# Kernel optimization log

Hardware: AMD Instinct MI355X
Metric: run time of the kernel (lower is better)

## Reference

```python
import jax, jax.numpy as jnp
import numpy as np

W_LOSS = 10.0
THRESHOLD = 1.0
ACOS_EPS = 1e-7


def _normalize(v, eps=1e-8):
    n = jnp.linalg.norm(v, axis=-1, keepdims=True)
    return v / jnp.maximum(n, eps)


def quat_to_rotmat(q):
    # q: (..., 4) in (w, x, y, z) order, as in Zhou et al. / EPN repo
    q = _normalize(q)
    w, x, y, z = q[..., 0], q[..., 1], q[..., 2], q[..., 3]
    R = jnp.stack([
        1 - 2 * (y * y + z * z), 2 * (x * y - z * w), 2 * (x * z + y * w),
        2 * (x * y + z * w), 1 - 2 * (x * x + z * z), 2 * (y * z - x * w),
        2 * (x * z - y * w), 2 * (y * z + x * w), 1 - 2 * (x * x + y * y),
    ], axis=-1)
    return R.reshape(q.shape[:-1] + (3, 3))


def acos_safe(x):
    return jnp.arccos(jnp.clip(x, -1.0 + ACOS_EPS, 1.0 - ACOS_EPS))


def angle_from_R(R):
    # R: (..., 3, 3) -> geodesic angle via trace
    tr = jnp.trace(R, axis1=-2, axis2=-1)
    return acos_safe(0.5 * (tr - 1.0))


def setup_inputs() -> dict:
    key = jax.random.key(0)
    k1, k2, k3, k4, k5 = jax.random.split(key, 5)
    B, NA, NR = 32768, 60, 4
    wts = jax.random.normal(k1, (B, NA), dtype=jnp.float32)
    label = jax.random.randint(k2, (B,), 0, NA, dtype=jnp.int64)
    y = jax.random.normal(k3, (B, NR, NA), dtype=jnp.float32)
    # gt_R and anchors are valid rotation matrices (via random quaternions)
    gt_R = quat_to_rotmat(jax.random.normal(k4, (B, NA, 4), dtype=jnp.float32))
    anchors = quat_to_rotmat(jax.random.normal(k5, (NA, 4), dtype=jnp.float32))
    return {"wts": wts, "label": label, "y": y, "gt_R": gt_R, "anchors": anchors}


def reference(wts, label, y, gt_R, anchors):
    b, na = wts.shape
    nr = y.shape[1]
    true_R = gt_R[:, 29]  # (b, 3, 3)

    # --- CrossEntropyLoss branch (classifier) ---
    logp = jax.nn.log_softmax(wts, axis=1)
    cls_loss = -jnp.mean(jnp.take_along_axis(logp, label[:, None], axis=1))
    preds = jnp.argmax(wts, axis=1)  # (b,)
    r_acc = jnp.mean((preds == label).astype(jnp.float32))

    # --- anchor-wise predicted rotations ---
    # y (b, nr, na) -> (b, na, nr) -> (b, na, 3, 3)
    pred_RAnchor = quat_to_rotmat(jnp.swapaxes(y, 1, 2))

    gt_bias = angle_from_R(gt_R)  # (b, na)
    mask = (gt_bias < THRESHOLD).astype(gt_R.dtype)[:, :, None, None]
    l2_loss = jnp.sum(jnp.square(gt_R * mask - pred_RAnchor * mask))
    loss = cls_loss + W_LOSS * l2_loss

    # --- final predicted rotation: gather best anchor, compose with anchor rot ---
    sel = jnp.take_along_axis(pred_RAnchor, preds[:, None, None, None], axis=1)[:, 0]  # (b,3,3)
    pred_R = jnp.einsum('bij,bjk->bik', anchors[preds], sel)

    # --- mean angular error ---
    ang_err = angle_from_R(jnp.einsum('bij,bkj->bik', pred_R, true_R))  # (b,)

    return (loss, cls_loss, W_LOSS * l2_loss, r_acc, ang_err)
```

## Files before the change

kernel.cpp:

```cpp
#include <hip/hip_runtime.h>
#include <math.h>

constexpr int Bc  = 32768;
constexpr int NAc = 60;
constexpr int NRc = 4;

constexpr int NP     = Bc * NAc;
constexpr int TILE   = 256;
constexpr int NTILES = NP / TILE;
constexpr int K1_BLOCKS = 3840;
constexpr int K2_BLOCKS = 1024;
constexpr int K2_WAVES  = K2_BLOCKS * 4;

#define COS_ONE 0.5403023058681398f

__global__ __launch_bounds__(256) void l2_pairs(
    const float* __restrict__ y,
    const float* __restrict__ gt_R,
    float*       __restrict__ l2p)
{
    __shared__ float4 sg4[TILE * 9 / 4];
    float* sg = (float*)sg4;
    const int tid = threadIdx.x;

    float acc = 0.0f;

    for (int tile = blockIdx.x; tile < NTILES; tile += gridDim.x) {
        __syncthreads();
        const float4* gbase = (const float4*)(gt_R + (size_t)tile * (TILE * 9));
        for (int i = tid; i < TILE * 9 / 4; i += 256) sg4[i] = gbase[i];
        __syncthreads();

        const int p = tile * TILE + tid;
        const int b = p / NAc;
        const int a = p - b * NAc;

        const float* yb = y + (size_t)b * (NRc * NAc) + a;
        float qw = yb[0 * NAc];
        float qx = yb[1 * NAc];
        float qy = yb[2 * NAc];
        float qz = yb[3 * NAc];

        const float* g = sg + tid * 9;
        float g0 = g[0], g1 = g[1], g2 = g[2];
        float g3 = g[3], g4 = g[4], g5 = g[5];
        float g6 = g[6], g7 = g[7], g8 = g[8];

        float n   = sqrtf(qw * qw + qx * qx + qy * qy + qz * qz);
        float inv = 1.0f / fmaxf(n, 1e-8f);
        qw *= inv; qx *= inv; qy *= inv; qz *= inv;

        float R00 = 1.0f - 2.0f * (qy * qy + qz * qz);
        float R01 = 2.0f * (qx * qy - qz * qw);
        float R02 = 2.0f * (qx * qz + qy * qw);
        float R10 = 2.0f * (qx * qy + qz * qw);
        float R11 = 1.0f - 2.0f * (qx * qx + qz * qz);
        float R12 = 2.0f * (qy * qz - qx * qw);
        float R20 = 2.0f * (qx * qz - qy * qw);
        float R21 = 2.0f * (qy * qz + qx * qw);
        float R22 = 1.0f - 2.0f * (qx * qx + qy * qy);

        float xb = 0.5f * (g0 + g4 + g8 - 1.0f);
        if (xb > COS_ONE) {
            float d0 = g0 - R00, d1 = g1 - R01, d2 = g2 - R02;
            float d3 = g3 - R10, d4 = g4 - R11, d5 = g5 - R12;
            float d6 = g6 - R20, d7 = g7 - R21, d8 = g8 - R22;
            acc += d0 * d0 + d1 * d1 + d2 * d2
                 + d3 * d3 + d4 * d4 + d5 * d5
                 + d6 * d6 + d7 * d7 + d8 * d8;
        }
    }

    for (int off = 32; off; off >>= 1) acc += __shfl_xor(acc, off, 64);
    __shared__ float sred[4];
    const int lane = tid & 63, wave = tid >> 6;
    if (lane == 0) sred[wave] = acc;
    __syncthreads();
    if (tid == 0) l2p[blockIdx.x] = sred[0] + sred[1] + sred[2] + sred[3];
}

__global__ __launch_bounds__(256) void cls_angerr(
    const float* __restrict__ wts,
    const int*   __restrict__ label,
    const float* __restrict__ y,
    const float* __restrict__ gt_R,
    const float* __restrict__ anchors,
    float*       __restrict__ out,
    float*       __restrict__ lpp,
    float*       __restrict__ crp)
{
    const int lane = threadIdx.x & 63;
    const int wave = threadIdx.x >> 6;
    const int gw   = blockIdx.x * 4 + wave;

    float lp_acc = 0.0f;
    float cr_acc = 0.0f;

    for (int b = gw; b < Bc; b += K2_WAVES) {
        float w = -INFINITY;
        if (lane < NAc) w = wts[(size_t)b * NAc + lane];
        float mv = w;
        int   mi = lane;
        for (int off = 32; off; off >>= 1) {
            float ov = __shfl_xor(mv, off, 64);
            int   oi = __shfl_xor(mi, off, 64);
            if (ov > mv || (ov == mv && oi < mi)) { mv = ov; mi = oi; }
        }
        float e  = (lane < NAc) ? expf(w - mv) : 0.0f;
        float se = e;
        for (int off = 32; off; off >>= 1) se += __shfl_xor(se, off, 64);
        float lse  = mv + logf(se);
        int   lab  = label[b];
        float wlab = __shfl(w, lab, 64);
        if (lane == 0) {
            lp_acc += wlab - lse;
            cr_acc += (mi == lab) ? 1.0f : 0.0f;
        }

        if (lane == mi) {
            const float* yb = y + (size_t)b * (NRc * NAc) + mi;
            float qw = yb[0 * NAc];
            float qx = yb[1 * NAc];
            float qy = yb[2 * NAc];
            float qz = yb[3 * NAc];
            float n   = sqrtf(qw * qw + qx * qx + qy * qy + qz * qz);
            float inv = 1.0f / fmaxf(n, 1e-8f);
            qw *= inv; qx *= inv; qy *= inv; qz *= inv;
            float R00 = 1.0f - 2.0f * (qy * qy + qz * qz);
            float R01 = 2.0f * (qx * qy - qz * qw);
            float R02 = 2.0f * (qx * qz + qy * qw);
            float R10 = 2.0f * (qx * qy + qz * qw);
            float R11 = 1.0f - 2.0f * (qx * qx + qz * qz);
            float R12 = 2.0f * (qy * qz - qx * qw);
            float R20 = 2.0f * (qx * qz - qy * qw);
            float R21 = 2.0f * (qy * qz + qx * qw);
            float R22 = 1.0f - 2.0f * (qx * qx + qy * qy);

            const float* A = anchors + (size_t)mi * 9;
            float a0 = A[0], a1 = A[1], a2 = A[2];
            float a3 = A[3], a4 = A[4], a5 = A[5];
            float a6 = A[6], a7 = A[7], a8 = A[8];
            float P00 = a0 * R00 + a1 * R10 + a2 * R20;
            float P01 = a0 * R01 + a1 * R11 + a2 * R21;
            float P02 = a0 * R02 + a1 * R12 + a2 * R22;
            float P10 = a3 * R00 + a4 * R10 + a5 * R20;
            float P11 = a3 * R01 + a4 * R11 + a5 * R21;
            float P12 = a3 * R02 + a4 * R12 + a5 * R22;
            float P20 = a6 * R00 + a7 * R10 + a8 * R20;
            float P21 = a6 * R01 + a7 * R11 + a8 * R21;
            float P22 = a6 * R02 + a7 * R12 + a8 * R22;
            const float* tR = gt_R + ((size_t)b * NAc + 29) * 9;
            float tr = P00 * tR[0] + P01 * tR[1] + P02 * tR[2]
                     + P10 * tR[3] + P11 * tR[4] + P12 * tR[5]
                     + P20 * tR[6] + P21 * tR[7] + P22 * tR[8];
            float cx = 0.5f * (tr - 1.0f);
            cx = fminf(fmaxf(cx, -1.0f + 1e-7f), 1.0f - 1e-7f);
            out[4 + b] = acosf(cx);
        }
    }

    for (int off = 32; off; off >>= 1) {
        lp_acc += __shfl_xor(lp_acc, off, 64);
        cr_acc += __shfl_xor(cr_acc, off, 64);
    }
    __shared__ float s_lp[4], s_cr[4];
    if (lane == 0) { s_lp[wave] = lp_acc; s_cr[wave] = cr_acc; }
    __syncthreads();
    if (threadIdx.x == 0) {
        lpp[blockIdx.x] = s_lp[0] + s_lp[1] + s_lp[2] + s_lp[3];
        crp[blockIdx.x] = s_cr[0] + s_cr[1] + s_cr[2] + s_cr[3];
    }
}

__global__ __launch_bounds__(64) void mtl_final(
    const float* __restrict__ l2p,
    const float* __restrict__ lpp,
    const float* __restrict__ crp,
    float*       __restrict__ out)
{
    const int lane = threadIdx.x;
    double l2 = 0.0, lp = 0.0, cr = 0.0;
    for (int i = lane; i < K1_BLOCKS; i += 64) l2 += (double)l2p[i];
    for (int i = lane; i < K2_BLOCKS; i += 64) {
        lp += (double)lpp[i];
        cr += (double)crp[i];
    }
    for (int off = 32; off; off >>= 1) {
        l2 += __shfl_xor(l2, off, 64);
        lp += __shfl_xor(lp, off, 64);
        cr += __shfl_xor(cr, off, 64);
    }
    if (lane == 0) {
        float cls = (float)(-lp / (double)Bc);
        float l2s = (float)(10.0 * l2);
        out[0] = cls + l2s;
        out[1] = cls;
        out[2] = l2s;
        out[3] = (float)(cr / (double)Bc);
    }
}

extern "C" void kernel_launch(void* const* d_in, const int* in_sizes, int n_in,
                              void* d_out, int out_size, void* d_ws, size_t ws_size,
                              hipStream_t stream) {
    const float* wts     = (const float*)d_in[0];
    const int*   label   = (const int*)d_in[1];
    const float* y       = (const float*)d_in[2];
    const float* gt_R    = (const float*)d_in[3];
    const float* anchors = (const float*)d_in[4];
    float* out = (float*)d_out;

    float* l2p = (float*)d_ws;
    float* lpp = l2p + K1_BLOCKS;
    float* crp = lpp + K2_BLOCKS;

    l2_pairs  <<<K1_BLOCKS, 256, 0, stream>>>(y, gt_R, l2p);
    cls_angerr<<<K2_BLOCKS, 256, 0, stream>>>(wts, label, y, gt_R, anchors, out, lpp, crp);
    mtl_final <<<1, 64, 0, stream>>>(l2p, lpp, crp, out);
}
```

Measured before the change: 172.2 us.

## Fuse L2 and classifier kernels into one grid with one tile per block

Merges the masked L2 kernel and the classifier/angle-error kernel into a single launch. Block ranges are split between the two roles, and the grid-stride loops are replaced by one tile (or four samples) per block. The y quaternion loads are issued before the shared-memory barrier so they overlap the gt_R tile staging. This removes one kernel launch and the serialization between the two stages, and lets both workloads share the GPU. In exchange, the partial-sum arrays in the final reduction grow to many more entries (7680 + 8192).

```diff
diff --git a/kernel.cpp b/kernel.cpp
--- a/kernel.cpp
+++ b/kernel.cpp
@@ -7,39 +7,46 @@
 
 constexpr int NP     = Bc * NAc;
 constexpr int TILE   = 256;
-constexpr int NTILES = NP / TILE;
-constexpr int K1_BLOCKS = 3840;
-constexpr int K2_BLOCKS = 1024;
-constexpr int K2_WAVES  = K2_BLOCKS * 4;
+constexpr int L2_BLOCKS  = NP / TILE;
+constexpr int CLS_BLOCKS = Bc / 4;
+constexpr int TOT_BLOCKS = L2_BLOCKS + CLS_BLOCKS;
 
 #define COS_ONE 0.5403023058681398f
 
-__global__ __launch_bounds__(256) void l2_pairs(
+__global__ __launch_bounds__(256) void mtl_fused(
+    const float* __restrict__ wts,
+    const int*   __restrict__ label,
     const float* __restrict__ y,
     const float* __restrict__ gt_R,
-    float*       __restrict__ l2p)
+    const float* __restrict__ anchors,
+    float*       __restrict__ out,
+    float*       __restrict__ l2p,
+    float*       __restrict__ lpp,
+    float*       __restrict__ crp)
 {
-    __shared__ float4 sg4[TILE * 9 / 4];
-    float* sg = (float*)sg4;
-    const int tid = threadIdx.x;
-
-    float acc = 0.0f;
-
-    for (int tile = blockIdx.x; tile < NTILES; tile += gridDim.x) {
-        __syncthreads();
+    const int tid  = threadIdx.x;
+    const int lane = tid & 63;
+    const int wave = tid >> 6;
+
+    if (blockIdx.x < L2_BLOCKS) {
+        __shared__ float4 sg4[TILE * 9 / 4];
+        float* sg = (float*)sg4;
+        const int tile = blockIdx.x;
+
         const float4* gbase = (const float4*)(gt_R + (size_t)tile * (TILE * 9));
-        for (int i = tid; i < TILE * 9 / 4; i += 256) sg4[i] = gbase[i];
-        __syncthreads();
+        sg4[tid] = gbase[tid];
+        sg4[tid + 256] = gbase[tid + 256];
+        if (tid < TILE * 9 / 4 - 512) sg4[tid + 512] = gbase[tid + 512];
 
         const int p = tile * TILE + tid;
         const int b = p / NAc;
         const int a = p - b * NAc;
-
         const float* yb = y + (size_t)b * (NRc * NAc) + a;
         float qw = yb[0 * NAc];
         float qx = yb[1 * NAc];
         float qy = yb[2 * NAc];
         float qz = yb[3 * NAc];
+        __syncthreads();
 
         const float* g = sg + tid * 9;
         float g0 = g[0], g1 = g[1], g2 = g[2];
@@ -60,43 +67,27 @@
         float R21 = 2.0f * (qy * qz + qx * qw);
         float R22 = 1.0f - 2.0f * (qx * qx + qy * qy);
 
+        float acc = 0.0f;
         float xb = 0.5f * (g0 + g4 + g8 - 1.0f);
         if (xb > COS_ONE) {
             float d0 = g0 - R00, d1 = g1 - R01, d2 = g2 - R02;
             float d3 = g3 - R10, d4 = g4 - R11, d5 = g5 - R12;
             float d6 = g6 - R20, d7 = g7 - R21, d8 = g8 - R22;
-            acc += d0 * d0 + d1 * d1 + d2 * d2
-                 + d3 * d3 + d4 * d4 + d5 * d5
-                 + d6 * d6 + d7 * d7 + d8 * d8;
-        }
-    }
-
-    for (int off = 32; off; off >>= 1) acc += __shfl_xor(acc, off, 64);
-    __shared__ float sred[4];
-    const int lane = tid & 63, wave = tid >> 6;
-    if (lane == 0) sred[wave] = acc;
-    __syncthreads();
-    if (tid == 0) l2p[blockIdx.x] = sred[0] + sred[1] + sred[2] + sred[3];
-}
-
-__global__ __launch_bounds__(256) void cls_angerr(
-    const float* __restrict__ wts,
-    const int*   __restrict__ label,
-    const float* __restrict__ y,
-    const float* __restrict__ gt_R,
-    const float* __restrict__ anchors,
-    float*       __restrict__ out,
-    float*       __restrict__ lpp,
-    float*       __restrict__ crp)
-{
-    const int lane = threadIdx.x & 63;
-    const int wave = threadIdx.x >> 6;
-    const int gw   = blockIdx.x * 4 + wave;
-
-    float lp_acc = 0.0f;
-    float cr_acc = 0.0f;
-
-    for (int b = gw; b < Bc; b += K2_WAVES) {
+            acc = d0 * d0 + d1 * d1 + d2 * d2
+                + d3 * d3 + d4 * d4 + d5 * d5
+                + d6 * d6 + d7 * d7 + d8 * d8;
+        }
+
+        for (int off = 32; off; off >>= 1) acc += __shfl_xor(acc, off, 64);
+        __shared__ float sred[4];
+        if (lane == 0) sred[wave] = acc;
+        __syncthreads();
+        if (tid == 0) l2p[tile] = sred[0] + sred[1] + sred[2] + sred[3];
+
+    } else {
+        const int cb = blockIdx.x - L2_BLOCKS;
+        const int b  = cb * 4 + wave;
+
         float w = -INFINITY;
         if (lane < NAc) w = wts[(size_t)b * NAc + lane];
         float mv = w;
@@ -112,17 +103,19 @@
         float lse  = mv + logf(se);
         int   lab  = label[b];
         float wlab = __shfl(w, lab, 64);
+
+        __shared__ float s_lp[4], s_cr[4];
         if (lane == 0) {
-            lp_acc += wlab - lse;
-            cr_acc += (mi == lab) ? 1.0f : 0.0f;
+            s_lp[wave] = wlab - lse;
+            s_cr[wave] = (mi == lab) ? 1.0f : 0.0f;
         }
 
         if (lane == mi) {
-            const float* yb = y + (size_t)b * (NRc * NAc) + mi;
-            float qw = yb[0 * NAc];
-            float qx = yb[1 * NAc];
-            float qy = yb[2 * NAc];
-            float qz = yb[3 * NAc];
+            const float* ybp = y + (size_t)b * (NRc * NAc) + mi;
+            float qw = ybp[0 * NAc];
+            float qx = ybp[1 * NAc];
+            float qy = ybp[2 * NAc];
+            float qz = ybp[3 * NAc];
             float n   = sqrtf(qw * qw + qx * qx + qy * qy + qz * qz);
             float inv = 1.0f / fmaxf(n, 1e-8f);
             qw *= inv; qx *= inv; qy *= inv; qz *= inv;
@@ -157,18 +150,12 @@
             cx = fminf(fmaxf(cx, -1.0f + 1e-7f), 1.0f - 1e-7f);
             out[4 + b] = acosf(cx);
         }
-    }
-
-    for (int off = 32; off; off >>= 1) {
-        lp_acc += __shfl_xor(lp_acc, off, 64);
-        cr_acc += __shfl_xor(cr_acc, off, 64);
-    }
-    __shared__ float s_lp[4], s_cr[4];
-    if (lane == 0) { s_lp[wave] = lp_acc; s_cr[wave] = cr_acc; }
-    __syncthreads();
-    if (threadIdx.x == 0) {
-        lpp[blockIdx.x] = s_lp[0] + s_lp[1] + s_lp[2] + s_lp[3];
-        crp[blockIdx.x] = s_cr[0] + s_cr[1] + s_cr[2] + s_cr[3];
+
+        __syncthreads();
+        if (tid == 0) {
+            lpp[cb] = s_lp[0] + s_lp[1] + s_lp[2] + s_lp[3];
+            crp[cb] = s_cr[0] + s_cr[1] + s_cr[2] + s_cr[3];
+        }
     }
 }
 
@@ -180,8 +167,8 @@
 {
     const int lane = threadIdx.x;
     double l2 = 0.0, lp = 0.0, cr = 0.0;
-    for (int i = lane; i < K1_BLOCKS; i += 64) l2 += (double)l2p[i];
-    for (int i = lane; i < K2_BLOCKS; i += 64) {
+    for (int i = lane; i < L2_BLOCKS; i += 64) l2 += (double)l2p[i];
+    for (int i = lane; i < CLS_BLOCKS; i += 64) {
         lp += (double)lpp[i];
         cr += (double)crp[i];
     }
@@ -211,10 +198,10 @@
     float* out = (float*)d_out;
 
     float* l2p = (float*)d_ws;
-    float* lpp = l2p + K1_BLOCKS;
-    float* crp = lpp + K2_BLOCKS;
-
-    l2_pairs  <<<K1_BLOCKS, 256, 0, stream>>>(y, gt_R, l2p);
-    cls_angerr<<<K2_BLOCKS, 256, 0, stream>>>(wts, label, y, gt_R, anchors, out, lpp, crp);
-    mtl_final <<<1, 64, 0, stream>>>(l2p, lpp, crp, out);
+    float* lpp = l2p + L2_BLOCKS;
+    float* crp = lpp + CLS_BLOCKS;
+
+    mtl_fused<<<TOT_BLOCKS, 256, 0, stream>>>(wts, label, y, gt_R, anchors,
+                                              out, l2p, lpp, crp);
+    mtl_final<<<1, 64, 0, stream>>>(l2p, lpp, crp, out);
 }
```

Measured after the change: 206.9 us. 1.2x slower.
